# Kernel tuning notes

Hardware: AMD Instinct MI355X
Metric: run time of the kernel (lower is better)

Reference implementation:

```python
import jax, jax.numpy as jnp
import numpy as np

VOCAB, H, K, Vd, O, L = 32000, 1024, 512, 1024, 1024, 2
B, T = 4, 1024


def setup_inputs() -> dict:
    key = jax.random.key(0)
    ks = jax.random.split(key, 14)
    s = 0.02
    return {
        "input_ids": jax.random.randint(ks[0], (B, T), 0, VOCAB, dtype=jnp.int64 if jax.config.jax_enable_x64 else jnp.int32).astype(jnp.int32),
        "emb": jax.random.normal(ks[1], (VOCAB, H), dtype=jnp.float32) * s,
        "Wq": jax.random.normal(ks[2], (L, H, K), dtype=jnp.float32) * s,
        "bq": jnp.zeros((L, K), dtype=jnp.float32),
        "Wk": jax.random.normal(ks[3], (L, H, K), dtype=jnp.float32) * s,
        "bk": jnp.zeros((L, K), dtype=jnp.float32),
        "Wg": jax.random.normal(ks[4], (L, H, K), dtype=jnp.float32) * s,
        "bg": jnp.zeros((L, K), dtype=jnp.float32),
        "Wv": jax.random.normal(ks[5], (L, H, Vd), dtype=jnp.float32) * s,
        "bv": jnp.zeros((L, Vd), dtype=jnp.float32),
        "Wo": jax.random.normal(ks[6], (L, Vd, O), dtype=jnp.float32) * s,
        "bo": jnp.zeros((L, O), dtype=jnp.float32),
        "W_head": jax.random.normal(ks[7], (O, VOCAB), dtype=jnp.float32) * s,
        "b_head": jnp.zeros((VOCAB,), dtype=jnp.float32),
    }


def _rnn_layer(h, Wq, bq, Wk, bk, Wg, bg, Wv, bv, Wo, bo):
    # h: (B, T, H). Project all timesteps at once (big GEMMs).
    q = h @ Wq + bq                      # (B,T,K)
    k = jax.nn.sigmoid(h @ Wk + bk)      # (B,T,K)
    g = jax.nn.sigmoid(h @ Wg + bg)      # (B,T,K)
    v = h @ Wv + bv                      # (B,T,Vd)

    def step(state, qkgv):
        q_t, k_t, g_t, v_t = qkgv        # each (B, K) or (B, Vd)
        state = state * g_t[:, :, None] + k_t[:, :, None] * v_t[:, None, :]
        out_t = jnp.einsum('bkv,bk->bv', state, q_t)
        return state, out_t

    init = jnp.zeros((h.shape[0], Wq.shape[1], Wv.shape[1]), dtype=h.dtype)  # (B,K,Vd)
    xs = (jnp.swapaxes(q, 0, 1), jnp.swapaxes(k, 0, 1),
          jnp.swapaxes(g, 0, 1), jnp.swapaxes(v, 0, 1))  # time-major
    state, outs = jax.lax.scan(step, init, xs)
    out = jnp.swapaxes(outs, 0, 1) @ Wo + bo  # (B,T,O)
    return out, state


def reference(input_ids, emb, Wq, bq, Wk, bk, Wg, bg, Wv, bv, Wo, bo, W_head, b_head):
    h = emb[input_ids]  # (B,T,H)
    for l in range(Wq.shape[0]):
        h, _ = _rnn_layer(h, Wq[l], bq[l], Wk[l], bk[l], Wg[l], bg[l],
                          Wv[l], bv[l], Wo[l], bo[l])
    logits = h @ W_head + b_head  # (B,T,VOCAB)
    return logits
```

## Files before the change

### kernel.cpp

```cpp
#include <hip/hip_runtime.h>
#include <hip/hip_bf16.h>

typedef unsigned short ushort;
typedef __attribute__((ext_vector_type(8))) short short8;
typedef __attribute__((ext_vector_type(4))) float floatx4;

#define TB   1024
#define BB   4
#define HH   1024
#define KK   512
#define VD   1024
#define OO   1024
#define NVOC 32000
#define NL   2
#define NTOK (BB*TB)
#define NHALF 16000

__device__ __forceinline__ float bf2f(ushort u) { return __uint_as_float(((unsigned)u) << 16); }
__device__ __forceinline__ ushort f2bf(float f) {
    unsigned x = __float_as_uint(f);
    return (ushort)((x + 0x7fffu + ((x >> 16) & 1u)) >> 16);
}

__device__ __forceinline__ void gld16(void* dst, const void* src) {
    __builtin_amdgcn_global_load_lds(
        (__attribute__((address_space(1))) void*)(void*)src,
        (__attribute__((address_space(3))) void*)dst, 16, 0, 0);
}

__global__ void probe_k(const ushort* __restrict__ emb, int* __restrict__ flag) {
    __shared__ int any;
    if (threadIdx.x == 0) any = 0;
    __syncthreads();
    int bad = 0;
    for (int i = threadIdx.x; i < 32768; i += 256) {
        float a = fabsf(bf2f(emb[i]));
        if (a > 1e6f) bad = 1;
    }
    if (bad) any = 1;
    __syncthreads();
    if (threadIdx.x == 0) *flag = any;
}

__global__ void cvt_bias_k(const void* __restrict__ src, ushort* __restrict__ dst, int n,
                           const int* __restrict__ flagp) {
    int i = blockIdx.x * 256 + threadIdx.x;
    if (i >= n) return;
    if (*flagp) dst[i] = f2bf(((const float*)src)[i]);
    else        dst[i] = ((const ushort*)src)[i];
}

__global__ __launch_bounds__(256) void transpose_k(const void* __restrict__ in_, size_t eoff,
                                                   ushort* __restrict__ out, int R, int C,
                                                   const int* __restrict__ flagp) {
    __shared__ ushort tile[32][33];
    const int bx = blockIdx.x * 32;
    const int by = blockIdx.y * 32;
    const int tx = threadIdx.x & 31;
    const int ty = threadIdx.x >> 5;
    if (*flagp) {
        const float* in = (const float*)in_ + eoff;
#pragma unroll
        for (int i = 0; i < 32; i += 8)
            tile[ty + i][tx] = f2bf(in[(size_t)(by + ty + i) * C + bx + tx]);
    } else {
        const ushort* in = (const ushort*)in_ + eoff;
#pragma unroll
        for (int i = 0; i < 32; i += 8)
            tile[ty + i][tx] = in[(size_t)(by + ty + i) * C + bx + tx];
    }
    __syncthreads();
#pragma unroll
    for (int i = 0; i < 32; i += 8)
        out[(size_t)(bx + ty + i) * R + by + tx] = tile[tx][ty + i];
}

__global__ __launch_bounds__(256) void gather_k(const int* __restrict__ ids,
                                                const void* __restrict__ emb_,
                                                ushort* __restrict__ h,
                                                const int* __restrict__ flagp) {
    int t = blockIdx.x;
    int id = ids[t];
    int c = threadIdx.x * 4;
    if (*flagp) {
        const float* emb = (const float*)emb_;
        float4 v = *(const float4*)&emb[(size_t)id * HH + c];
        ushort4 o; o.x = f2bf(v.x); o.y = f2bf(v.y); o.z = f2bf(v.z); o.w = f2bf(v.w);
        *(ushort4*)&h[(size_t)t * HH + c] = o;
    } else {
        const ushort* emb = (const ushort*)emb_;
        *(uint2*)&h[(size_t)t * HH + c] = *(const uint2*)&emb[(size_t)id * HH + c];
    }
}

template<int MODE>
__global__ __launch_bounds__(256) void gemm_bt(
    const ushort* __restrict__ A, const ushort* __restrict__ Bt, void* __restrict__ Cv,
    const ushort* __restrict__ b0, const ushort* __restrict__ b1,
    const ushort* __restrict__ b2, const ushort* __restrict__ b3,
    int K, int ldc, int coloff, const int* __restrict__ flagp)
{
    __shared__ ushort As[128][32];
    __shared__ ushort Bs[128][32];

    const int tid  = threadIdx.x;
    const int bm   = blockIdx.y * 128;
    const int bn   = blockIdx.x * 128;
    const int wave = tid >> 6, lane = tid & 63;
    const int wm   = (wave >> 1) * 64, wn = (wave & 1) * 64;
    const int l15  = lane & 15, quad = lane >> 4;

    floatx4 acc[4][4];
#pragma unroll
    for (int i = 0; i < 4; i++)
#pragma unroll
        for (int j = 0; j < 4; j++) acc[i][j] = (floatx4){0.f, 0.f, 0.f, 0.f};

    const int srow = wave * 16 + (lane >> 2);
    const int scol = (lane & 3) * 8;
    const ushort* aS0 = A  + (size_t)(bm + srow) * K + scol;
    const ushort* aS1 = aS0 + (size_t)64 * K;
    const ushort* bS0 = Bt + (size_t)(bn + srow) * K + scol;
    const ushort* bS1 = bS0 + (size_t)64 * K;
    ushort* aD0 = &As[wave * 16][0];
    ushort* aD1 = &As[64 + wave * 16][0];
    ushort* bD0 = &Bs[wave * 16][0];
    ushort* bD1 = &Bs[64 + wave * 16][0];

    for (int kt = 0; kt < K; kt += 32) {
        gld16(aD0, aS0 + kt);
        gld16(aD1, aS1 + kt);
        gld16(bD0, bS0 + kt);
        gld16(bD1, bS1 + kt);
        __syncthreads();

        short8 af[4], bfr[4];
#pragma unroll
        for (int i = 0; i < 4; i++) af[i]  = *(const short8*)&As[wm + i * 16 + l15][quad * 8];
#pragma unroll
        for (int i = 0; i < 4; i++) bfr[i] = *(const short8*)&Bs[wn + i * 16 + l15][quad * 8];
#pragma unroll
        for (int i = 0; i < 4; i++)
#pragma unroll
            for (int j = 0; j < 4; j++)
                acc[i][j] = __builtin_amdgcn_mfma_f32_16x16x32_bf16(af[i], bfr[j], acc[i][j], 0, 0, 0);
        __syncthreads();
    }

    const int f = (MODE == 2) ? *flagp : 0;

#pragma unroll
    for (int i = 0; i < 4; i++) {
#pragma unroll
        for (int j = 0; j < 4; j++) {
            const int col = bn + wn + j * 16 + l15;
            float bias; bool sig = false;
            if (MODE == 1) {
                if      (col < KK)     { bias = bf2f(b0[col]); }
                else if (col < 2 * KK) { bias = bf2f(b1[col - KK]);     sig = true; }
                else if (col < 3 * KK) { bias = bf2f(b2[col - 2 * KK]); sig = true; }
                else                   { bias = bf2f(b3[col - 3 * KK]); }
            } else {
                bias = bf2f(b0[col]);
            }
#pragma unroll
            for (int r = 0; r < 4; r++) {
                const int row = bm + wm + i * 16 + quad * 4 + r;
                float v = acc[i][j][r] + bias;
                if (sig) v = 1.f / (1.f + __expf(-v));
                const size_t idx = (size_t)row * ldc + coloff + col;
                if (MODE == 1)      ((float*)Cv)[idx]  = v;
                else if (MODE == 0) ((ushort*)Cv)[idx] = f2bf(v);
                else { if (f) ((float*)Cv)[idx] = v; else ((ushort*)Cv)[idx] = f2bf(v); }
            }
        }
    }
}

__device__ __forceinline__ int qslot(int i4) {
    const int hi = i4 >> 3, lo = i4 & 7;
    return hi * 32 + ((4 * (lo + hi)) & 31);
}

__global__ __launch_bounds__(256) void scan_k(const float* __restrict__ qkgv,
                                              ushort* __restrict__ outp)
{
    const int b   = blockIdx.y;
    const int v0  = blockIdx.x * 16;
    const int tid = threadIdx.x;
    const int lane = tid & 63;
    const int wave = tid >> 6;
    const int kg   = lane >> 2;
    const int vl   = lane & 3;
    const int kb   = kg * 32;
    const int vloc = wave * 4 + vl;
    const int myv  = v0 + vloc;

    __shared__ float sq[3][512], sk[3][512], sg[3][512];
    __shared__ float sv[3][16];

    float s[32];
#pragma unroll
    for (int j = 0; j < 32; j++) s[j] = 0.f;

    const size_t rowbase = (size_t)b * TB * 2560;

    const int slot0 = qslot(tid & 127);
    const int off0  = (tid < 128) ? tid * 4 : 512 + (tid - 128) * 4;
    const int off1  = (tid < 128) ? 1024 + tid * 4 : 1536 + v0 + (tid - 128) * 4;

    float4 A0 = {0,0,0,0}, A1 = {0,0,0,0}, A2 = {0,0,0,0};
    float4 B0 = {0,0,0,0}, B1 = {0,0,0,0}, B2 = {0,0,0,0};

    {
        const float* r0 = qkgv + rowbase;
        A0 = *(const float4*)&r0[off0];
        A1 = *(const float4*)&r0[2560 + off0];
        A2 = *(const float4*)&r0[5120 + off0];
        if (tid < 132) {
            B0 = *(const float4*)&r0[off1];
            B1 = *(const float4*)&r0[2560 + off1];
            B2 = *(const float4*)&r0[5120 + off1];
        }
        float* dqk = (tid < 128) ? &sq[0][0] : &sk[0][0];
        *(float4*)&dqk[slot0] = A0;
        if (tid < 132) {
            if (tid < 128) *(float4*)&sg[0][slot0] = B0;
            else           *(float4*)&sv[0][(tid - 128) * 4] = B0;
        }
        __syncthreads();
    }

#define SCAN_STEP(T, RW_A, RW_B, RL_A, RL_B, BW_, BC_)                              \
    {                                                                               \
        const int t_ = (T);                                                         \
        if (t_ + 1 < TB) {                                                          \
            float* dqk_ = (tid < 128) ? &sq[BW_][0] : &sk[BW_][0];                  \
            *(float4*)&dqk_[slot0] = RW_A;                                          \
            if (tid < 132) {                                                        \
                if (tid < 128) *(float4*)&sg[BW_][slot0] = RW_B;                    \
                else           *(float4*)&sv[BW_][(tid - 128) * 4] = RW_B;          \
            }                                                                       \
        }                                                                           \
        if (t_ + 3 < TB) {                                                          \
            const float* row_ = qkgv + rowbase + (size_t)(t_ + 3) * 2560;           \
            RL_A = *(const float4*)&row_[off0];                                     \
            if (tid < 132) RL_B = *(const float4*)&row_[off1];                      \
        }                                                                           \
        if (t_ < TB) {                                                              \
            const float vv = sv[BC_][vloc];                                         \
            float po = 0.f;                                                         \
            _Pragma("unroll")                                                       \
            for (int m = 0; m < 8; m++) {                                           \
                const int off = ((m + kg) * 4) & 31;                                \
                float4 g4 = *(const float4*)&sg[BC_][kb + off];                     \
                float4 k4 = *(const float4*)&sk[BC_][kb + off];                     \
                float4 q4 = *(const float4*)&sq[BC_][kb + off];                     \
                s[m*4+0] = fmaf(s[m*4+0], g4.x, k4.x * vv); po = fmaf(q4.x, s[m*4+0], po); \
                s[m*4+1] = fmaf(s[m*4+1], g4.y, k4.y * vv); po = fmaf(q4.y, s[m*4+1], po); \
                s[m*4+2] = fmaf(s[m*4+2], g4.z, k4.z * vv); po = fmaf(q4.z, s[m*4+2], po); \
                s[m*4+3] = fmaf(s[m*4+3], g4.w, k4.w * vv); po = fmaf(q4.w, s[m*4+3], po); \
            }                                                                       \
            po += __shfl_xor(po, 4, 64);                                            \
            po += __shfl_xor(po, 8, 64);                                            \
            po += __shfl_xor(po, 16, 64);                                           \
            po += __shfl_xor(po, 32, 64);                                           \
            if (kg == 0) outp[((size_t)b * TB + t_) * VD + myv] = f2bf(po);         \
        }                                                                           \
        __syncthreads();                                                            \
    }

    for (int t = 0; t < TB; t += 3) {
        SCAN_STEP(t,     A1, B1, A0, B0, 1, 0);
        SCAN_STEP(t + 1, A2, B2, A1, B1, 2, 1);
        SCAN_STEP(t + 2, A0, B0, A2, B2, 0, 2);
    }
#undef SCAN_STEP
}

extern "C" void kernel_launch(void* const* d_in, const int* in_sizes, int n_in,
                              void* d_out, int out_size, void* d_ws, size_t ws_size,
                              hipStream_t stream) {
    const int*  ids = (const int*)d_in[0];
    const void* emb = d_in[1];
    const void* Wq  = d_in[2];
    const void* bq  = d_in[3];
    const void* Wk  = d_in[4];
    const void* bk  = d_in[5];
    const void* Wg  = d_in[6];
    const void* bg  = d_in[7];
    const void* Wv  = d_in[8];
    const void* bv  = d_in[9];
    const void* Wo  = d_in[10];
    const void* bo  = d_in[11];
    const void* Wh  = d_in[12];
    const void* bh  = d_in[13];
    (void)in_sizes; (void)n_in; (void)out_size; (void)ws_size;

    char* p = (char*)d_ws;
    auto alloc = [&](size_t bytes) { char* r = p; p += (bytes + 255) & ~(size_t)255; return (void*)r; };
    int*    flagp = (int*)alloc(4);
    ushort* biasc = (ushort*)alloc((size_t)39168 * 2);
    ushort* bqc = biasc, *bkc = biasc + 1024, *bgc = biasc + 2048;
    ushort* bvc = biasc + 3072, *boc = biasc + 5120, *bhc = biasc + 7168;
    ushort* Wcat  = (ushort*)alloc((size_t)NL * 2560 * HH * 2);
    ushort* Wot   = (ushort*)alloc((size_t)NL * OO * VD * 2);
    ushort* h     = (ushort*)alloc((size_t)NTOK * HH * 2);
    ushort* Whalf = (ushort*)alloc((size_t)NHALF * OO * 2);

    float*  qkgv  = (float*)d_out;
    ushort* scano = (ushort*)((char*)d_out + (size_t)NTOK * 2560 * 4);

    probe_k<<<1, 256, 0, stream>>>((const ushort*)emb, flagp);
    cvt_bias_k<<<(NL*KK + 255) / 256, 256, 0, stream>>>(bq, bqc, NL*KK, flagp);
    cvt_bias_k<<<(NL*KK + 255) / 256, 256, 0, stream>>>(bk, bkc, NL*KK, flagp);
    cvt_bias_k<<<(NL*KK + 255) / 256, 256, 0, stream>>>(bg, bgc, NL*KK, flagp);
    cvt_bias_k<<<(NL*VD + 255) / 256, 256, 0, stream>>>(bv, bvc, NL*VD, flagp);
    cvt_bias_k<<<(NL*OO + 255) / 256, 256, 0, stream>>>(bo, boc, NL*OO, flagp);
    cvt_bias_k<<<(NVOC  + 255) / 256, 256, 0, stream>>>(bh, bhc, NVOC,  flagp);

    for (int l = 0; l < NL; l++) {
        ushort* Wc = Wcat + (size_t)l * 2560 * HH;
        transpose_k<<<dim3(KK/32, HH/32), 256, 0, stream>>>(Wq, (size_t)l*HH*KK, Wc,                   HH, KK, flagp);
        transpose_k<<<dim3(KK/32, HH/32), 256, 0, stream>>>(Wk, (size_t)l*HH*KK, Wc + (size_t)KK*HH,   HH, KK, flagp);
        transpose_k<<<dim3(KK/32, HH/32), 256, 0, stream>>>(Wg, (size_t)l*HH*KK, Wc + (size_t)2*KK*HH, HH, KK, flagp);
        transpose_k<<<dim3(VD/32, HH/32), 256, 0, stream>>>(Wv, (size_t)l*HH*VD, Wc + (size_t)3*KK*HH, HH, VD, flagp);
        transpose_k<<<dim3(OO/32, VD/32), 256, 0, stream>>>(Wo, (size_t)l*VD*OO, Wot + (size_t)l*OO*VD, VD, OO, flagp);
    }

    gather_k<<<NTOK, 256, 0, stream>>>(ids, emb, h, flagp);

    for (int l = 0; l < NL; l++) {
        const ushort* Wc = Wcat + (size_t)l * 2560 * HH;
        gemm_bt<1><<<dim3(2560/128, NTOK/128), 256, 0, stream>>>(
            h, Wc, qkgv, bqc + l*KK, bkc + l*KK, bgc + l*KK, bvc + l*VD,
            HH, 2560, 0, flagp);
        scan_k<<<dim3(VD/16, BB), 256, 0, stream>>>(qkgv, scano);
        gemm_bt<0><<<dim3(OO/128, NTOK/128), 256, 0, stream>>>(
            scano, Wot + (size_t)l*OO*VD, h, boc + l*OO, nullptr, nullptr, nullptr,
            VD, OO, 0, flagp);
    }

    for (int c0 = 0; c0 < NVOC; c0 += NHALF) {
        transpose_k<<<dim3(NHALF/32, OO/32), 256, 0, stream>>>(Wh, (size_t)c0, Whalf, OO, NVOC, flagp);
        gemm_bt<2><<<dim3(NHALF/128, NTOK/128), 256, 0, stream>>>(
            h, Whalf, d_out, bhc + c0, nullptr, nullptr, nullptr,
            OO, NVOC, c0, flagp);
    }
}
```

Measured before the change: 2.549 ms.

## Split scan across two K-halves and combine partial outputs

```diff
diff --git a/kernel.cpp b/kernel.cpp
--- a/kernel.cpp
+++ b/kernel.cpp
@@ -177,105 +177,114 @@
     }
 }
 
-__device__ __forceinline__ int qslot(int i4) {
-    const int hi = i4 >> 3, lo = i4 & 7;
-    return hi * 32 + ((4 * (lo + hi)) & 31);
-}
-
-__global__ __launch_bounds__(256) void scan_k(const float* __restrict__ qkgv,
-                                              ushort* __restrict__ outp)
+__global__ __launch_bounds__(256, 2) void scan_k(const float* __restrict__ qkgv,
+                                                 float* __restrict__ pout)
 {
-    const int b   = blockIdx.y;
-    const int v0  = blockIdx.x * 16;
-    const int tid = threadIdx.x;
+    const int b    = blockIdx.y;
+    const int v0   = blockIdx.x * 16;
+    const int kz   = blockIdx.z;
+    const int tid  = threadIdx.x;
     const int lane = tid & 63;
     const int wave = tid >> 6;
     const int kg   = lane >> 2;
     const int vl   = lane & 3;
-    const int kb   = kg * 32;
     const int vloc = wave * 4 + vl;
     const int myv  = v0 + vloc;
 
-    __shared__ float sq[3][512], sk[3][512], sg[3][512];
-    __shared__ float sv[3][16];
-
-    float s[32];
-#pragma unroll
-    for (int j = 0; j < 32; j++) s[j] = 0.f;
+    __shared__ float sq[3][256], sk[3][256], sg[3][256], sv[3][16];
+
+    float s[16];
+#pragma unroll
+    for (int j = 0; j < 16; j++) s[j] = 0.f;
 
     const size_t rowbase = (size_t)b * TB * 2560;
 
-    const int slot0 = qslot(tid & 127);
-    const int off0  = (tid < 128) ? tid * 4 : 512 + (tid - 128) * 4;
-    const int off1  = (tid < 128) ? 1024 + tid * 4 : 1536 + v0 + (tid - 128) * 4;
-
-    float4 A0 = {0,0,0,0}, A1 = {0,0,0,0}, A2 = {0,0,0,0};
-    float4 B0 = {0,0,0,0}, B1 = {0,0,0,0}, B2 = {0,0,0,0};
+    const int  srole = wave;
+    const bool sact  = (srole < 3) || (lane < 4);
+    const int  goff  = (srole < 3) ? srole * 512 + kz * 256 + lane * 4
+                                   : 1536 + v0 + lane * 4;
+    const int  slotf = (srole < 3) ? ((lane & 3) * 16 + (lane >> 2)) * 4
+                                   : lane * 4;
+
+    float4 R0 = {0,0,0,0}, R1 = {0,0,0,0}, R2 = {0,0,0,0};
 
     {
         const float* r0 = qkgv + rowbase;
-        A0 = *(const float4*)&r0[off0];
-        A1 = *(const float4*)&r0[2560 + off0];
-        A2 = *(const float4*)&r0[5120 + off0];
-        if (tid < 132) {
-            B0 = *(const float4*)&r0[off1];
-            B1 = *(const float4*)&r0[2560 + off1];
-            B2 = *(const float4*)&r0[5120 + off1];
+        if (sact) {
+            R0 = *(const float4*)&r0[goff];
+            R1 = *(const float4*)&r0[2560 + goff];
+            R2 = *(const float4*)&r0[5120 + goff];
         }
-        float* dqk = (tid < 128) ? &sq[0][0] : &sk[0][0];
-        *(float4*)&dqk[slot0] = A0;
-        if (tid < 132) {
-            if (tid < 128) *(float4*)&sg[0][slot0] = B0;
-            else           *(float4*)&sv[0][(tid - 128) * 4] = B0;
-        }
+        if (srole == 0)      *(float4*)&sq[0][slotf] = R0;
+        else if (srole == 1) *(float4*)&sk[0][slotf] = R0;
+        else if (srole == 2) *(float4*)&sg[0][slotf] = R0;
+        else if (lane < 4)   *(float4*)&sv[0][slotf] = R0;
         __syncthreads();
     }
 
-#define SCAN_STEP(T, RW_A, RW_B, RL_A, RL_B, BW_, BC_)                              \
+#define SCAN_STEP(T, RW, RL, BW_, BC_)                                              \
     {                                                                               \
         const int t_ = (T);                                                         \
         if (t_ + 1 < TB) {                                                          \
-            float* dqk_ = (tid < 128) ? &sq[BW_][0] : &sk[BW_][0];                  \
-            *(float4*)&dqk_[slot0] = RW_A;                                          \
-            if (tid < 132) {                                                        \
-                if (tid < 128) *(float4*)&sg[BW_][slot0] = RW_B;                    \
-                else           *(float4*)&sv[BW_][(tid - 128) * 4] = RW_B;          \
-            }                                                                       \
+            if (srole == 0)      *(float4*)&sq[BW_][slotf] = RW;                    \
+            else if (srole == 1) *(float4*)&sk[BW_][slotf] = RW;                    \
+            else if (srole == 2) *(float4*)&sg[BW_][slotf] = RW;                    \
+            else if (lane < 4)   *(float4*)&sv[BW_][slotf] = RW;                    \
         }                                                                           \
-        if (t_ + 3 < TB) {                                                          \
+        if (t_ + 3 < TB && sact) {                                                  \
             const float* row_ = qkgv + rowbase + (size_t)(t_ + 3) * 2560;           \
-            RL_A = *(const float4*)&row_[off0];                                     \
-            if (tid < 132) RL_B = *(const float4*)&row_[off1];                      \
+            RL = *(const float4*)&row_[goff];                                       \
         }                                                                           \
         if (t_ < TB) {                                                              \
             const float vv = sv[BC_][vloc];                                         \
-            float po = 0.f;                                                         \
+            float po0, po1, po2, po3;                                               \
             _Pragma("unroll")                                                       \
-            for (int m = 0; m < 8; m++) {                                           \
-                const int off = ((m + kg) * 4) & 31;                                \
-                float4 g4 = *(const float4*)&sg[BC_][kb + off];                     \
-                float4 k4 = *(const float4*)&sk[BC_][kb + off];                     \
-                float4 q4 = *(const float4*)&sq[BC_][kb + off];                     \
-                s[m*4+0] = fmaf(s[m*4+0], g4.x, k4.x * vv); po = fmaf(q4.x, s[m*4+0], po); \
-                s[m*4+1] = fmaf(s[m*4+1], g4.y, k4.y * vv); po = fmaf(q4.y, s[m*4+1], po); \
-                s[m*4+2] = fmaf(s[m*4+2], g4.z, k4.z * vv); po = fmaf(q4.z, s[m*4+2], po); \
-                s[m*4+3] = fmaf(s[m*4+3], g4.w, k4.w * vv); po = fmaf(q4.w, s[m*4+3], po); \
+            for (int m = 0; m < 4; m++) {                                           \
+                const int off = m * 64 + kg * 4;                                    \
+                float4 g4 = *(const float4*)&sg[BC_][off];                          \
+                float4 k4 = *(const float4*)&sk[BC_][off];                          \
+                float4 q4 = *(const float4*)&sq[BC_][off];                          \
+                float* sm = &s[m * 4];                                              \
+                sm[0] = fmaf(sm[0], g4.x, k4.x * vv);                               \
+                sm[1] = fmaf(sm[1], g4.y, k4.y * vv);                               \
+                sm[2] = fmaf(sm[2], g4.z, k4.z * vv);                               \
+                sm[3] = fmaf(sm[3], g4.w, k4.w * vv);                               \
+                float pm;                                                           \
+                pm = q4.x * sm[0];                                                  \
+                pm = fmaf(q4.y, sm[1], pm);                                         \
+                pm = fmaf(q4.z, sm[2], pm);                                         \
+                pm = fmaf(q4.w, sm[3], pm);                                         \
+                if (m == 0) po0 = pm; else if (m == 1) po1 = pm;                    \
+                else if (m == 2) po2 = pm; else po3 = pm;                           \
             }                                                                       \
+            float po = (po0 + po1) + (po2 + po3);                                   \
             po += __shfl_xor(po, 4, 64);                                            \
             po += __shfl_xor(po, 8, 64);                                            \
             po += __shfl_xor(po, 16, 64);                                           \
             po += __shfl_xor(po, 32, 64);                                           \
-            if (kg == 0) outp[((size_t)b * TB + t_) * VD + myv] = f2bf(po);         \
+            if (kg == 0)                                                            \
+                pout[(((size_t)kz * BB + b) * TB + t_) * VD + myv] = po;            \
         }                                                                           \
         __syncthreads();                                                            \
     }
 
     for (int t = 0; t < TB; t += 3) {
-        SCAN_STEP(t,     A1, B1, A0, B0, 1, 0);
-        SCAN_STEP(t + 1, A2, B2, A1, B1, 2, 1);
-        SCAN_STEP(t + 2, A0, B0, A2, B2, 0, 2);
+        SCAN_STEP(t,     R1, R0, 1, 0);
+        SCAN_STEP(t + 1, R2, R1, 2, 1);
+        SCAN_STEP(t + 2, R0, R2, 0, 2);
     }
 #undef SCAN_STEP
+}
+
+__global__ __launch_bounds__(256) void combine_k(const float* __restrict__ pout,
+                                                 ushort* __restrict__ outp) {
+    const size_t i = ((size_t)blockIdx.x * 256 + threadIdx.x) * 4;
+    float4 a = *(const float4*)&pout[i];
+    float4 c = *(const float4*)&pout[(size_t)NTOK * VD + i];
+    ushort4 o;
+    o.x = f2bf(a.x + c.x); o.y = f2bf(a.y + c.y);
+    o.z = f2bf(a.z + c.z); o.w = f2bf(a.w + c.w);
+    *(ushort4*)&outp[i] = o;
 }
 
 extern "C" void kernel_launch(void* const* d_in, const int* in_sizes, int n_in,
@@ -310,6 +319,8 @@
 
     float*  qkgv  = (float*)d_out;
     ushort* scano = (ushort*)((char*)d_out + (size_t)NTOK * 2560 * 4);
+    float*  pout  = (float*)((char*)d_out + (size_t)NTOK * 2560 * 4
+                                          + (size_t)NTOK * VD * 2);
 
     probe_k<<<1, 256, 0, stream>>>((const ushort*)emb, flagp);
     cvt_bias_k<<<(NL*KK + 255) / 256, 256, 0, stream>>>(bq, bqc, NL*KK, flagp);
@@ -335,7 +346,8 @@
         gemm_bt<1><<<dim3(2560/128, NTOK/128), 256, 0, stream>>>(
             h, Wc, qkgv, bqc + l*KK, bkc + l*KK, bgc + l*KK, bvc + l*VD,
             HH, 2560, 0, flagp);
-        scan_k<<<dim3(VD/16, BB), 256, 0, stream>>>(qkgv, scano);
+        scan_k<<<dim3(VD/16, BB, 2), 256, 0, stream>>>(qkgv, pout);
+        combine_k<<<(NTOK * VD / 4) / 256, 256, 0, stream>>>(pout, scano);
         gemm_bt<0><<<dim3(OO/128, NTOK/128), 256, 0, stream>>>(
             scano, Wot + (size_t)l*OO*VD, h, boc + l*OO, nullptr, nullptr, nullptr,
             VD, OO, 0, flagp);
```

Result: faster. 2.450 ms (-3.9%).
